# Kernel optimization log

Hardware: AMD Instinct MI355X
Metric: run time of the kernel (lower is better)

## Reference

```python
import jax, jax.numpy as jnp
import numpy as np

S = 4            # scale_factor (conv-transpose stride)
K = 5            # kernel_size
PAD = 1 + (K - S - 1) // 2   # = 1
OP = (K - S) % 2             # = 1 (output_padding)
SCALE_SPACE = 0.1
SCALE_COLOR = 0.5


def setup_inputs() -> dict:
    key = jax.random.key(0)
    k1, k2 = jax.random.split(key)
    x = jax.random.normal(k1, (4, 1, 128, 128), dtype=jnp.float32)
    hr_guidance = jax.random.uniform(k2, (4, 3, 512, 512), dtype=jnp.float32)
    # convt.weight after __init__ fill: identity across channels, all-ones over KxK window
    weight = jnp.ones((1, 1, K, K), dtype=jnp.float32)
    return {"x": x, "hr_guidance": hr_guidance, "weight": weight}


def _valid_1d(n):
    # Indicator over the padded, stride-inserted axis (length n+K-1): positions that
    # hold real low-res samples (mask_pattern of packernel2d, transposed nd2col of ones).
    pad_lo = (K - 1) - PAD
    n_lo = (n + 2 * PAD - OP - (K - 1) - 1) // S + 1   # back-computed low-res size
    n_up = (n_lo - 1) * S + 1                          # stride-inserted size
    idx = jnp.arange(n + K - 1) - pad_lo
    return ((idx >= 0) & (idx < n_up) & (idx % S == 0)).astype(jnp.float32)


def _bilateral_kernel(G):
    # G: (bs, C, H, W) scaled guidance features -> normalized PAC kernel (bs, K*K, H, W)
    bs, C, H, W = G.shape
    r = (K - 1) // 2                                   # guidance unfold padding (k-1)*d//2
    Gp = jnp.pad(G, ((0, 0), (0, 0), (r, r), (r, r)))
    # gaussian of guidance differences; the center-tap feature equals G itself
    kern = jnp.stack([jnp.exp(-0.5 * jnp.sum((Gp[:, :, i:i + H, j:j + W] - G) ** 2, axis=1))
                      for i in range(K) for j in range(K)], axis=1)   # (bs, K*K, H, W)
    mh, mw = _valid_1d(H), _valid_1d(W)
    mask = jnp.stack([mh[i:i + H][:, None] * mw[j:j + W][None, :]
                      for i in range(K) for j in range(K)], axis=0)   # (K*K, H, W)
    kern = kern * mask[None]
    norm = jnp.sum(kern, axis=1, keepdims=True)        # normalize_kernel=True
    return kern / (norm + (norm == 0).astype(kern.dtype))


def _upsample_pad(x, H, W):
    # zero-insertion by stride S plus the padding conv_transpose implies
    bs, ch, h, w = x.shape
    pad_lo = (K - 1) - PAD
    Xp = jnp.zeros((bs, ch, H + K - 1, W + K - 1), x.dtype)
    return Xp.at[:, :, pad_lo:pad_lo + S * (h - 1) + 1:S,
                 pad_lo:pad_lo + S * (w - 1) + 1:S].set(x)


def reference(x, hr_guidance, weight):
    bs, cg, H, W = hr_guidance.shape
    hh = jnp.arange(H, dtype=hr_guidance.dtype)
    ww = jnp.arange(W, dtype=hr_guidance.dtype)
    G = jnp.concatenate([
        hr_guidance * SCALE_COLOR,
        jnp.broadcast_to(hh[None, None, :, None] * SCALE_SPACE, (bs, 1, H, W)),
        jnp.broadcast_to(ww[None, None, None, :] * SCALE_SPACE, (bs, 1, H, W)),
    ], axis=1)                                         # (bs, cg+2, H, W)
    kern = _bilateral_kernel(G)                        # (bs, K*K, H, W)
    Xp = _upsample_pad(x, H, W)
    cols = jnp.stack([Xp[:, 0, i:i + H, j:j + W]
                      for i in range(K) for j in range(K)], axis=1)   # (bs, K*K, H, W)
    # conv_transpose weight -> correlation weight: swap in/out channels, flip taps
    w_flat = weight.transpose(1, 0, 2, 3)[:, :, ::-1, ::-1].reshape(-1)  # (K*K,)
    out = jnp.einsum('bkhw,k->bhw', kern * cols, w_flat)
    return out[:, None]                                # (bs, 1, H, W)
```

## Files before the change

kernel.cpp:

```cpp
#include <hip/hip_runtime.h>


#define HW_ (512 * 512)

__global__ __launch_bounds__(256) void jbu_kernel(
    const float* __restrict__ x,
    const float* __restrict__ guide,
    const float* __restrict__ weight,
    float* __restrict__ out)
{
    int tid = blockIdx.x * blockDim.x + threadIdx.x;
    int m = tid & 127;
    int h = (tid >> 7) & 511;
    int b = tid >> 16;
    int q = h >> 2, rh = h & 3;

    const float* gb = guide + (size_t)b * 3 * HW_;
    const float* xb = x + b * 128 * 128;

    int cbase = h * 512 + 4 * m;
    float4 c0 = *(const float4*)(gb + cbase);
    float4 c1 = *(const float4*)(gb + HW_ + cbase);
    float4 c2 = *(const float4*)(gb + 2 * HW_ + cbase);
    float cc0[4] = {c0.x, c0.y, c0.z, c0.w};
    float cc1[4] = {c1.x, c1.y, c1.z, c1.w};
    float cc2[4] = {c2.x, c2.y, c2.z, c2.w};

    bool cs = (m < 127);
    int  co = cs ? 4 : 0;
    int  xo = cs ? 1 : 0;
    float csf = cs ? 1.0f : 0.0f;

    int sr = (4 * q + 1) * 512 + 4 * m + 1;
    float s00_0 = gb[sr],      s00_1 = gb[HW_ + sr],      s00_2 = gb[2 * HW_ + sr];
    float s01_0 = gb[sr + co], s01_1 = gb[HW_ + sr + co], s01_2 = gb[2 * HW_ + sr + co];
    float x00 = xb[q * 128 + m];
    float x01 = xb[q * 128 + m + xo];

    int dip = ((3 - rh) & 3) - 2;
    float spr0 = 0.005f * (float)(dip * dip);
    const float spcl[4] = {0.005f, 0.0f, 0.005f, 0.02f};

    int i0wi = rh + 1;
    float wr0[5], wr1[5];
    #pragma unroll
    for (int k = 0; k < 5; ++k) { wr0[k] = weight[i0wi * 5 + k]; wr1[k] = weight[k]; }

    float acc[4] = {0, 0, 0, 0}, nrm[4] = {0, 0, 0, 0};

    #pragma unroll
    for (int p = 0; p < 4; ++p) {
        float d0 = s00_0 - cc0[p], d1 = s00_1 - cc1[p], d2 = s00_2 - cc2[p];
        float kv = __expf(-0.125f * (d0*d0 + d1*d1 + d2*d2) - spr0 - spcl[p]) * wr0[p + 1];
        nrm[p] += kv; acc[p] += kv * x00;
    }
    {
        float d0 = s01_0 - cc0[3], d1 = s01_1 - cc1[3], d2 = s01_2 - cc2[3];
        float kv = __expf(-0.125f * (d0*d0 + d1*d1 + d2*d2) - spr0 - 0.02f) * wr0[0] * csf;
        nrm[3] += kv; acc[3] += kv * x01;
    }

    if (rh == 3 && q < 127) {
        int sr1 = sr + 4 * 512;
        float s10_0 = gb[sr1],      s10_1 = gb[HW_ + sr1],      s10_2 = gb[2 * HW_ + sr1];
        float s11_0 = gb[sr1 + co], s11_1 = gb[HW_ + sr1 + co], s11_2 = gb[2 * HW_ + sr1 + co];
        float x10 = xb[(q + 1) * 128 + m];
        float x11 = xb[(q + 1) * 128 + m + xo];
        #pragma unroll
        for (int p = 0; p < 4; ++p) {
            float d0 = s10_0 - cc0[p], d1 = s10_1 - cc1[p], d2 = s10_2 - cc2[p];
            float kv = __expf(-0.125f * (d0*d0 + d1*d1 + d2*d2) - 0.02f - spcl[p]) * wr1[p + 1];
            nrm[p] += kv; acc[p] += kv * x10;
        }
        float d0 = s11_0 - cc0[3], d1 = s11_1 - cc1[3], d2 = s11_2 - cc2[3];
        float kv = __expf(-0.125f * (d0*d0 + d1*d1 + d2*d2) - 0.04f) * wr1[0] * csf;
        nrm[3] += kv; acc[3] += kv * x11;
    }

    float4 o;
    o.x = acc[0] / nrm[0];
    o.y = acc[1] / nrm[1];
    o.z = acc[2] / nrm[2];
    o.w = acc[3] / nrm[3];
    *(float4*)(out + (size_t)b * HW_ + cbase) = o;
}

extern "C" void kernel_launch(void* const* d_in, const int* in_sizes, int n_in,
                              void* d_out, int out_size, void* d_ws, size_t ws_size,
                              hipStream_t stream) {
    const float* x      = (const float*)d_in[0];
    const float* guide  = (const float*)d_in[1];
    const float* weight = (const float*)d_in[2];
    float* out = (float*)d_out;

    (void)in_sizes; (void)n_in; (void)out_size; (void)d_ws; (void)ws_size;
    int total = 4 * 512 * 128;
    jbu_kernel<<<total / 256, 256, 0, stream>>>(x, guide, weight, out);
}
```

Baseline: 69.39 us.

## Compute a 4x4 output tile per thread to reuse sample-point loads

Each thread now handles a 4-row by 4-column output tile instead of one row of four pixels. The low-res samples and the guidance values at sample points are loaded once per tile and reused across all four rows, removing redundant scattered loads. This cuts the thread count by four, which lowers occupancy and parallelism for latency hiding, and raises register use to hold the 48 guidance values.

```diff
diff --git a/kernel.cpp b/kernel.cpp
--- a/kernel.cpp
+++ b/kernel.cpp
@@ -3,7 +3,7 @@
 
 #define HW_ (512 * 512)
 
-__global__ __launch_bounds__(256) void jbu_kernel(
+__global__ __launch_bounds__(256) void jbu_tile_kernel(
     const float* __restrict__ x,
     const float* __restrict__ guide,
     const float* __restrict__ weight,
@@ -11,78 +11,100 @@
 {
     int tid = blockIdx.x * blockDim.x + threadIdx.x;
     int m = tid & 127;
-    int h = (tid >> 7) & 511;
-    int b = tid >> 16;
-    int q = h >> 2, rh = h & 3;
+    int q = (tid >> 7) & 127;
+    int b = tid >> 14;
 
     const float* gb = guide + (size_t)b * 3 * HW_;
     const float* xb = x + b * 128 * 128;
 
-    int cbase = h * 512 + 4 * m;
-    float4 c0 = *(const float4*)(gb + cbase);
-    float4 c1 = *(const float4*)(gb + HW_ + cbase);
-    float4 c2 = *(const float4*)(gb + 2 * HW_ + cbase);
-    float cc0[4] = {c0.x, c0.y, c0.z, c0.w};
-    float cc1[4] = {c1.x, c1.y, c1.z, c1.w};
-    float cc2[4] = {c2.x, c2.y, c2.z, c2.w};
+    float c[3][4][4];
+    #pragma unroll
+    for (int ch = 0; ch < 3; ++ch)
+        #pragma unroll
+        for (int r = 0; r < 4; ++r) {
+            float4 v = *(const float4*)(gb + ch * HW_ + (4 * q + r) * 512 + 4 * m);
+            c[ch][r][0] = v.x; c[ch][r][1] = v.y; c[ch][r][2] = v.z; c[ch][r][3] = v.w;
+        }
 
-    bool cs = (m < 127);
-    int  co = cs ? 4 : 0;
-    int  xo = cs ? 1 : 0;
-    float csf = cs ? 1.0f : 0.0f;
+    bool cs = (m < 127), rs = (q < 127);
+    float csf = cs ? 1.0f : 0.0f, rsf = rs ? 1.0f : 0.0f;
+    int co = cs ? 4 : 0;
+    int ro = rs ? 4 * 512 : 0;
+    int xo = cs ? 1 : 0;
+    int xr = rs ? 128 : 0;
 
     int sr = (4 * q + 1) * 512 + 4 * m + 1;
-    float s00_0 = gb[sr],      s00_1 = gb[HW_ + sr],      s00_2 = gb[2 * HW_ + sr];
-    float s01_0 = gb[sr + co], s01_1 = gb[HW_ + sr + co], s01_2 = gb[2 * HW_ + sr + co];
+    float s00[3], s01[3], s10[3], s11[3];
+    #pragma unroll
+    for (int ch = 0; ch < 3; ++ch) {
+        s00[ch] = c[ch][1][1];
+        s01[ch] = gb[ch * HW_ + sr + co];
+        s10[ch] = gb[ch * HW_ + sr + ro];
+        s11[ch] = gb[ch * HW_ + sr + ro + co];
+    }
     float x00 = xb[q * 128 + m];
     float x01 = xb[q * 128 + m + xo];
+    float x10 = xb[q * 128 + m + xr];
+    float x11 = xb[q * 128 + m + xr + xo];
 
-    int dip = ((3 - rh) & 3) - 2;
-    float spr0 = 0.005f * (float)(dip * dip);
-    const float spcl[4] = {0.005f, 0.0f, 0.005f, 0.02f};
+    float w_[25];
+    #pragma unroll
+    for (int k = 0; k < 6; ++k) {
+        float4 v = *(const float4*)(weight + 4 * k);
+        w_[4 * k] = v.x; w_[4 * k + 1] = v.y; w_[4 * k + 2] = v.z; w_[4 * k + 3] = v.w;
+    }
+    w_[24] = weight[24];
 
-    int i0wi = rh + 1;
-    float wr0[5], wr1[5];
-    #pragma unroll
-    for (int k = 0; k < 5; ++k) { wr0[k] = weight[i0wi * 5 + k]; wr1[k] = weight[k]; }
+    const float sp[4] = {0.005f, 0.0f, 0.005f, 0.02f};
 
-    float acc[4] = {0, 0, 0, 0}, nrm[4] = {0, 0, 0, 0};
+    size_t obase = (size_t)b * HW_ + (size_t)(4 * q) * 512 + 4 * m;
 
     #pragma unroll
-    for (int p = 0; p < 4; ++p) {
-        float d0 = s00_0 - cc0[p], d1 = s00_1 - cc1[p], d2 = s00_2 - cc2[p];
-        float kv = __expf(-0.125f * (d0*d0 + d1*d1 + d2*d2) - spr0 - spcl[p]) * wr0[p + 1];
-        nrm[p] += kv; acc[p] += kv * x00;
-    }
-    {
-        float d0 = s01_0 - cc0[3], d1 = s01_1 - cc1[3], d2 = s01_2 - cc2[3];
-        float kv = __expf(-0.125f * (d0*d0 + d1*d1 + d2*d2) - spr0 - 0.02f) * wr0[0] * csf;
-        nrm[3] += kv; acc[3] += kv * x01;
-    }
+    for (int r = 0; r < 4; ++r) {
+        float acc[4] = {0, 0, 0, 0}, nrm[4] = {0, 0, 0, 0};
 
-    if (rh == 3 && q < 127) {
-        int sr1 = sr + 4 * 512;
-        float s10_0 = gb[sr1],      s10_1 = gb[HW_ + sr1],      s10_2 = gb[2 * HW_ + sr1];
-        float s11_0 = gb[sr1 + co], s11_1 = gb[HW_ + sr1 + co], s11_2 = gb[2 * HW_ + sr1 + co];
-        float x10 = xb[(q + 1) * 128 + m];
-        float x11 = xb[(q + 1) * 128 + m + xo];
         #pragma unroll
         for (int p = 0; p < 4; ++p) {
-            float d0 = s10_0 - cc0[p], d1 = s10_1 - cc1[p], d2 = s10_2 - cc2[p];
-            float kv = __expf(-0.125f * (d0*d0 + d1*d1 + d2*d2) - 0.02f - spcl[p]) * wr1[p + 1];
-            nrm[p] += kv; acc[p] += kv * x10;
+            float d0 = s00[0] - c[0][r][p];
+            float d1 = s00[1] - c[1][r][p];
+            float d2 = s00[2] - c[2][r][p];
+            float t = d0 * d0 + d1 * d1 + d2 * d2;
+            float kv = __expf(-0.125f * t - sp[r] - sp[p]) * w_[(r + 1) * 5 + p + 1];
+            nrm[p] += kv; acc[p] += kv * x00;
         }
-        float d0 = s11_0 - cc0[3], d1 = s11_1 - cc1[3], d2 = s11_2 - cc2[3];
-        float kv = __expf(-0.125f * (d0*d0 + d1*d1 + d2*d2) - 0.04f) * wr1[0] * csf;
-        nrm[3] += kv; acc[3] += kv * x11;
+        {
+            float d0 = s01[0] - c[0][r][3];
+            float d1 = s01[1] - c[1][r][3];
+            float d2 = s01[2] - c[2][r][3];
+            float t = d0 * d0 + d1 * d1 + d2 * d2;
+            float kv = __expf(-0.125f * t - sp[r] - 0.02f) * w_[(r + 1) * 5] * csf;
+            nrm[3] += kv; acc[3] += kv * x01;
+        }
+        if (r == 3) {
+            #pragma unroll
+            for (int p = 0; p < 4; ++p) {
+                float d0 = s10[0] - c[0][3][p];
+                float d1 = s10[1] - c[1][3][p];
+                float d2 = s10[2] - c[2][3][p];
+                float t = d0 * d0 + d1 * d1 + d2 * d2;
+                float kv = __expf(-0.125f * t - 0.02f - sp[p]) * w_[p + 1] * rsf;
+                nrm[p] += kv; acc[p] += kv * x10;
+            }
+            float d0 = s11[0] - c[0][3][3];
+            float d1 = s11[1] - c[1][3][3];
+            float d2 = s11[2] - c[2][3][3];
+            float t = d0 * d0 + d1 * d1 + d2 * d2;
+            float kv = __expf(-0.125f * t - 0.04f) * w_[0] * (rsf * csf);
+            nrm[3] += kv; acc[3] += kv * x11;
+        }
+
+        float4 o;
+        o.x = acc[0] / nrm[0];
+        o.y = acc[1] / nrm[1];
+        o.z = acc[2] / nrm[2];
+        o.w = acc[3] / nrm[3];
+        *(float4*)(out + obase + (size_t)r * 512) = o;
     }
-
-    float4 o;
-    o.x = acc[0] / nrm[0];
-    o.y = acc[1] / nrm[1];
-    o.z = acc[2] / nrm[2];
-    o.w = acc[3] / nrm[3];
-    *(float4*)(out + (size_t)b * HW_ + cbase) = o;
 }
 
 extern "C" void kernel_launch(void* const* d_in, const int* in_sizes, int n_in,
@@ -94,6 +116,6 @@
     float* out = (float*)d_out;
 
     (void)in_sizes; (void)n_in; (void)out_size; (void)d_ws; (void)ws_size;
-    int total = 4 * 512 * 128;
-    jbu_kernel<<<total / 256, 256, 0, stream>>>(x, guide, weight, out);
+    int total = 4 * 128 * 128;
+    jbu_tile_kernel<<<total / 256, 256, 0, stream>>>(x, guide, weight, out);
 }
```

Result: faster. 67.50 us (-2.7%).
